# Kernel tuning notes

Measured on AMD Instinct MI355X. Metric: run time of the kernel, lower is better.

Reference implementation:

```python
import jax, jax.numpy as jnp
from jax import lax
import numpy as np

CONF_THRESH = 0.015
NMS_DIST = 4
BORDER = 4
RED = 8


def setup_inputs() -> dict:
    key = jax.random.key(0)
    k1, k2, k3, k4, k5 = jax.random.split(key, 5)
    B, C, H, W = 32, 128, 64, 64
    MID, NCLS = 256, RED * RED + 1
    return {
        "x": jax.random.normal(k1, (B, C, H, W), dtype=jnp.float32),
        "w1": jax.random.normal(k2, (MID, C, 3, 3), dtype=jnp.float32) * 0.05,
        "b1": jax.random.normal(k3, (MID,), dtype=jnp.float32) * 0.05,
        "w2": jax.random.normal(k4, (NCLS, MID, 1, 1), dtype=jnp.float32) * 0.05,
        "b2": jax.random.normal(k5, (NCLS,), dtype=jnp.float32) * 0.05,
    }


def _conv3x3(x, w, b):
    y = lax.conv_general_dilated(
        x, w, window_strides=(1, 1), padding="SAME",
        dimension_numbers=("NCHW", "OIHW", "NCHW"))
    return y + b[None, :, None, None]


def _max_pool(s, r):
    # s: [B, H, W]; infinity-norm neighborhood max, window (2r+1)x(2r+1)
    return lax.reduce_window(
        s, -jnp.inf, lax.max,
        window_dimensions=(1, 2 * r + 1, 2 * r + 1),
        window_strides=(1, 1, 1), padding="SAME")


def _grid_nms(scores, r, iters=8):
    # Iterated local-max suppression; converges to the greedy (sorted-by-score)
    # grid NMS of the original nms_fast routine for distinct scores.
    zeros = jnp.zeros_like(scores)
    max_mask = (scores == _max_pool(scores, r)) & (scores > 0)
    for _ in range(iters):
        supp = _max_pool(max_mask.astype(scores.dtype), r) > 0
        supp_scores = jnp.where(supp, zeros, scores)
        new_max = (supp_scores == _max_pool(supp_scores, r)) & (supp_scores > 0)
        max_mask = max_mask | (new_max & ~supp)
    return jnp.where(max_mask, scores, zeros)


def reference(x, w1, b1, w2, b2):
    B, _, hh, ww = x.shape
    h = jax.nn.relu(_conv3x3(x, w1, b1))                       # [B, mid, hh, ww]
    semi = jnp.einsum("bchw,oc->bohw", h, w2[:, :, 0, 0]) + b2[None, :, None, None]
    dense = jax.nn.softmax(semi, axis=1)                        # [B, 65, hh, ww]
    nodust = dense[:, :-1]                                      # drop dust bin
    # depth-to-space: [B,64,hh,ww] -> [B, hh*8, ww*8]
    heat = nodust.transpose(0, 2, 3, 1).reshape(B, hh, ww, RED, RED)
    heat = heat.transpose(0, 1, 3, 2, 4).reshape(B, hh * RED, ww * RED)
    # confidence threshold
    scores = jnp.where(heat >= CONF_THRESH, heat, 0.0)
    # grid-based NMS (dense keep-map formulation of nms_fast)
    kept = _grid_nms(scores, NMS_DIST)
    # border removal
    Hi, Wi = hh * RED, ww * RED
    yy = jnp.arange(Hi)
    xx = jnp.arange(Wi)
    border = ((yy[:, None] >= BORDER) & (yy[:, None] < Hi - BORDER) &
              (xx[None, :] >= BORDER) & (xx[None, :] < Wi - BORDER))
    return kept * border[None, :, :].astype(kept.dtype)
```

## Files before the change

### kernel.cpp

```cpp
#include <hip/hip_runtime.h>
#include <hip/hip_bf16.h>
#include <stdint.h>

#define BATCH 32
#define CIN 128
#define HH 64
#define WW 64
#define MID 256
#define NCLS 65
#define HI 512
#define NWORDS 8
#define XPS 136
#define HBS2 264
#define SEMS 68

typedef _Float16 half8 __attribute__((ext_vector_type(8)));
typedef _Float16 half4v __attribute__((ext_vector_type(4)));
typedef _Float16 half2v __attribute__((ext_vector_type(2)));
typedef float f32x4 __attribute__((ext_vector_type(4)));

__global__ __launch_bounds__(256) void prep_w1f(
    const float* __restrict__ w1, _Float16* __restrict__ w1fh,
    _Float16* __restrict__ w1fl)
{
    const int idx = blockIdx.x * 256 + threadIdx.x;
    const int j = idx & 7, lane = (idx >> 3) & 63, mt = (idx >> 9) & 15;
    const int s = (idx >> 13) & 3, kix = idx >> 15;
    const int m = mt * 16 + (lane & 15);
    const int c = s * 32 + (lane >> 4) * 8 + j;
    const int ky = kix / 3, kx = kix - ky * 3;
    const float v = w1[((m * CIN + c) * 3 + ky) * 3 + kx];
    const _Float16 hi = (_Float16)v;
    w1fh[idx] = hi;
    w1fl[idx] = (_Float16)(v - (float)hi);
}

__global__ __launch_bounds__(256) void prep_w2f(
    const float* __restrict__ w2, _Float16* __restrict__ w2fh,
    _Float16* __restrict__ w2fl)
{
    const int idx = blockIdx.x * 256 + threadIdx.x;
    const int j = idx & 7, lane = (idx >> 3) & 63;
    const int ks = (idx >> 9) & 7, mt = idx >> 12;
    const int o = mt * 16 + (lane & 15);
    const int k = ks * 32 + (lane >> 4) * 8 + j;
    const float v = (o < NCLS) ? w2[o * MID + k] : 0.f;
    const _Float16 hi = (_Float16)v;
    w2fh[idx] = hi;
    w2fl[idx] = (_Float16)(v - (float)hi);
}

__global__ __launch_bounds__(256) void head_kernel(
    const float* __restrict__ x,
    const _Float16* __restrict__ w1fh, const _Float16* __restrict__ w1fl,
    const _Float16* __restrict__ w2fh, const _Float16* __restrict__ w2fl,
    const float* __restrict__ b1, const float* __restrict__ b2,
    float* __restrict__ out)
{
    const int b  = blockIdx.z;
    const int y0 = blockIdx.y * 8, x0 = blockIdx.x * 8;
    const int tid = threadIdx.x;
    const int lane = tid & 63, w = tid >> 6;
    const int n = lane & 15, q = lane >> 4;

    __shared__ __align__(16) unsigned char SM[54400];
    _Float16* const xh = (_Float16*)SM;
    _Float16* const xl = xh + 100 * XPS;
    _Float16* const hbh = (_Float16*)SM;
    _Float16* const hbl = hbh + 32 * HBS2;
    float* const sem  = (float*)(SM + 33792);
    float* const rinv = sem + 32 * SEMS;

    const float* xb = x + (size_t)b * CIN * HH * WW;
    for (int i = tid; i < 6400; i += 256) {
        const int c2 = i / 100, pos = i - c2 * 100;
        const int r = pos / 10, cc = pos - r * 10;
        const int gy = y0 - 1 + r, gx = x0 - 1 + cc;
        const int c = c2 * 2;
        float v0 = 0.f, v1 = 0.f;
        if ((unsigned)gy < HH && (unsigned)gx < WW) {
            const float* p = xb + (c * HH + gy) * WW + gx;
            v0 = p[0]; v1 = p[HH * WW];
        }
        const _Float16 h0 = (_Float16)v0, h1 = (_Float16)v1;
        half2v hi = {h0, h1};
        half2v lo = {(_Float16)(v0 - (float)h0), (_Float16)(v1 - (float)h1)};
        *(half2v*)(xh + pos * XPS + c) = hi;
        *(half2v*)(xl + pos * XPS + c) = lo;
    }
    __syncthreads();

    f32x4 acc[4][4];
#pragma unroll
    for (int i = 0; i < 4; ++i)
#pragma unroll
        for (int t = 0; t < 4; ++t) acc[i][t] = (f32x4){0.f, 0.f, 0.f, 0.f};

    int bposT[4];
#pragma unroll
    for (int t = 0; t < 4; ++t)
        bposT[t] = (t * 2 + (n >> 3)) * 10 + (n & 7);

    for (int kix = 0; kix < 9; ++kix) {
        const int ky = kix / 3;
        const int koff = ky * 10 + (kix - ky * 3);
#pragma unroll
        for (int s = 0; s < 4; ++s) {
            half8 Ah[4], Al[4];
#pragma unroll
            for (int i = 0; i < 4; ++i) {
                const size_t o = (size_t)(kix * 4 + s) * 8192 +
                                 (w * 4 + i) * 512 + lane * 8;
                Ah[i] = *(const half8*)(w1fh + o);
                Al[i] = *(const half8*)(w1fl + o);
            }
            half8 Bh[4], Bl[4];
#pragma unroll
            for (int t = 0; t < 4; ++t) {
                const int a = (bposT[t] + koff) * XPS + s * 32 + q * 8;
                Bh[t] = *(const half8*)(xh + a);
                Bl[t] = *(const half8*)(xl + a);
            }
#pragma unroll
            for (int i = 0; i < 4; ++i)
#pragma unroll
                for (int t = 0; t < 4; ++t) {
                    acc[i][t] = __builtin_amdgcn_mfma_f32_16x16x32_f16(
                        Ah[i], Bh[t], acc[i][t], 0, 0, 0);
                    acc[i][t] = __builtin_amdgcn_mfma_f32_16x16x32_f16(
                        Ah[i], Bl[t], acc[i][t], 0, 0, 0);
                    acc[i][t] = __builtin_amdgcn_mfma_f32_16x16x32_f16(
                        Al[i], Bh[t], acc[i][t], 0, 0, 0);
                }
        }
    }
    __syncthreads();

    for (int hf = 0; hf < 2; ++hf) {
        if (hf) __syncthreads();
#pragma unroll
        for (int i = 0; i < 4; ++i)
#pragma unroll
            for (int tt = 0; tt < 2; ++tt) {
                const int t = hf * 2 + tt;
                const int p = tt * 16 + n;
                const int m0 = w * 64 + i * 16 + q * 4;
                const f32x4 a = acc[i][t];
                const float4 bv = *(const float4*)(b1 + m0);
                const float h0 = fmaxf(a[0] + bv.x, 0.f);
                const float h1 = fmaxf(a[1] + bv.y, 0.f);
                const float h2 = fmaxf(a[2] + bv.z, 0.f);
                const float h3 = fmaxf(a[3] + bv.w, 0.f);
                half4v hh = {(_Float16)h0, (_Float16)h1,
                             (_Float16)h2, (_Float16)h3};
                half4v hl = {(_Float16)(h0 - (float)hh[0]),
                             (_Float16)(h1 - (float)hh[1]),
                             (_Float16)(h2 - (float)hh[2]),
                             (_Float16)(h3 - (float)hh[3])};
                *(half4v*)(hbh + p * HBS2 + m0) = hh;
                *(half4v*)(hbl + p * HBS2 + m0) = hl;
            }
        __syncthreads();
        {
            const int nt = w & 1;
            const int mt0 = (w < 2) ? 0 : 3;
            const int nmt = (w < 2) ? 3 : 2;
            const int pb = nt * 16 + n;
            f32x4 a2[3];
#pragma unroll
            for (int j = 0; j < 3; ++j) a2[j] = (f32x4){0.f, 0.f, 0.f, 0.f};
#pragma unroll
            for (int ks = 0; ks < 8; ++ks) {
                const int ad = pb * HBS2 + ks * 32 + q * 8;
                const half8 B2h = *(const half8*)(hbh + ad);
                const half8 B2l = *(const half8*)(hbl + ad);
#pragma unroll
                for (int j = 0; j < 3; ++j)
                    if (j < nmt) {
                        const size_t o = (size_t)((mt0 + j) * 8 + ks) * 512 +
                                         lane * 8;
                        const half8 A2h = *(const half8*)(w2fh + o);
                        const half8 A2l = *(const half8*)(w2fl + o);
                        a2[j] = __builtin_amdgcn_mfma_f32_16x16x32_f16(
                            A2h, B2h, a2[j], 0, 0, 0);
                        a2[j] = __builtin_amdgcn_mfma_f32_16x16x32_f16(
                            A2h, B2l, a2[j], 0, 0, 0);
                        a2[j] = __builtin_amdgcn_mfma_f32_16x16x32_f16(
                            A2l, B2h, a2[j], 0, 0, 0);
                    }
            }
#pragma unroll
            for (int j = 0; j < 3; ++j)
                if (j < nmt) {
                    const int o0 = (mt0 + j) * 16 + q * 4;
#pragma unroll
                    for (int r2 = 0; r2 < 4; ++r2) {
                        const int o = o0 + r2;
                        if (o < NCLS)
                            sem[pb * SEMS + o] = a2[j][r2] + b2[o];
                    }
                }
        }
        __syncthreads();
        if (tid < 128) {
            const int p = tid >> 2, q4 = tid & 3;
            const int o0 = q4 * 17;
            const int o1 = (o0 + 17 < NCLS) ? o0 + 17 : NCLS;
            float mx = -1e30f;
            for (int o = o0; o < o1; ++o)
                mx = fmaxf(mx, sem[p * SEMS + o]);
            mx = fmaxf(mx, __shfl_xor(mx, 1));
            mx = fmaxf(mx, __shfl_xor(mx, 2));
            float ssum = 0.f;
            for (int o = o0; o < o1; ++o) {
                float e = __expf(sem[p * SEMS + o] - mx);
                sem[p * SEMS + o] = e;
                ssum += e;
            }
            ssum += __shfl_xor(ssum, 1);
            ssum += __shfl_xor(ssum, 2);
            if (q4 == 0) rinv[p] = 1.f / ssum;
        }
        __syncthreads();
        for (int t2 = tid; t2 < 2048; t2 += 256) {
            const int p = t2 >> 6, o = t2 & 63;
            float v = sem[p * SEMS + o] * rinv[p];
            if (!(v >= 0.015f)) v = 0.f;
            const int P = hf * 32 + p;
            const int py = P >> 3, px = P & 7;
            const int row = (y0 + py) * 8 + (o >> 3);
            const int col = (x0 + px) * 8 + (o & 7);
            out[((size_t)b * HI + row) * HI + col] = v;
        }
    }
}

__global__ __launch_bounds__(256) void nms_iter(
    const float* __restrict__ S, const uint64_t* __restrict__ Min,
    uint64_t* __restrict__ Mout)
{
    const int b = blockIdx.z;
    const int bx = blockIdx.x;
    const int ty = blockIdx.y * 64, tx = bx * 64;
    const int tid = threadIdx.x;

    __shared__ uint64_t smw[80 * 3];
    __shared__ uint64_t hd[80 * 3];
    __shared__ uint64_t sup[72 * 3];
    __shared__ __align__(16) float sfl[72 * 76];
    __shared__ __align__(16) float rm[72 * 64];

    if (tid < 240) {
        const int i = tid / 3, j = tid % 3;
        const int yy = ty - 8 + i;
        const int wj = bx - 1 + j;
        uint64_t v = 0;
        if (Min && (unsigned)yy < HI && (unsigned)wj < NWORDS)
            v = Min[((size_t)b * HI + yy) * NWORDS + wj];
        smw[tid] = v;
    }
    __syncthreads();
    if (tid < 240) {
        const int i = tid / 3, j = tid % 3;
        const uint64_t c = smw[i * 3 + j];
        const uint64_t l = j > 0 ? smw[i * 3 + j - 1] : 0ull;
        const uint64_t r = j < 2 ? smw[i * 3 + j + 1] : 0ull;
        uint64_t d = c;
#pragma unroll
        for (int s = 1; s <= 4; ++s)
            d |= (c >> s) | (r << (64 - s)) | (c << s) | (l >> (64 - s));
        hd[tid] = d;
    }
    __syncthreads();
    if (tid < 216) {
        const int r = tid / 3, j = tid % 3;
        uint64_t v = 0;
#pragma unroll
        for (int k = 0; k < 9; ++k) v |= hd[(r + k) * 3 + j];
        sup[tid] = v;
    }
    __syncthreads();
    const float* Sb = S + (size_t)b * HI * HI;
    for (int k = tid; k < 72 * 18; k += 256) {
        const int r = k / 18, f4 = k % 18;
        const int gy = ty - 4 + r;
        const int gx0 = tx - 4 + f4 * 4;
        float4 v = make_float4(0.f, 0.f, 0.f, 0.f);
        float* pv = (float*)&v;
        if ((unsigned)gy < HI) {
            if (gx0 >= 0 && gx0 + 3 < HI)
                v = *(const float4*)(Sb + (size_t)gy * HI + gx0);
            else {
#pragma unroll
                for (int cc = 0; cc < 4; ++cc)
                    if ((unsigned)(gx0 + cc) < HI)
                        pv[cc] = Sb[(size_t)gy * HI + gx0 + cc];
            }
        }
        const int rel64 = 60 + 4 * f4;
        const uint64_t w = sup[r * 3 + (rel64 >> 6)];
        const int b0 = rel64 & 63;
#pragma unroll
        for (int cc = 0; cc < 4; ++cc)
            if ((w >> (b0 + cc)) & 1ull) pv[cc] = 0.f;
        *(float4*)(sfl + r * 76 + f4 * 4) = v;
    }
    __syncthreads();
    for (int k = tid; k < 72 * 16; k += 256) {
        const int r = k / 16, x4 = (k % 16) * 4;
        const float4 a  = *(const float4*)(sfl + r * 76 + x4);
        const float4 bq = *(const float4*)(sfl + r * 76 + x4 + 4);
        const float4 cq = *(const float4*)(sfl + r * 76 + x4 + 8);
        const float v0=a.x,v1=a.y,v2=a.z,v3=a.w;
        const float v4=bq.x,v5=bq.y,v6=bq.z,v7=bq.w;
        const float v8=cq.x,v9=cq.y,v10=cq.z,v11=cq.w;
        const float m4567 = fmaxf(fmaxf(v4,v5), fmaxf(v6,v7));
        const float m23 = fmaxf(v2,v3), m89 = fmaxf(v8,v9);
        const float o0 = fmaxf(fmaxf(fmaxf(v0,v1), m23), fmaxf(m4567, v8));
        const float o1 = fmaxf(fmaxf(v1, m23), fmaxf(m4567, m89));
        const float o2 = fmaxf(fmaxf(m23, m4567), fmaxf(m89, v10));
        const float o3 = fmaxf(fmaxf(v3, m4567), fmaxf(fmaxf(m89, v10), v11));
        *(float4*)(rm + r * 64 + x4) = make_float4(o0,o1,o2,o3);
    }
    __syncthreads();
    {
        const int wv = tid >> 6, lane = tid & 63;
        const int ybase = wv * 16;
        float ring[9];
#pragma unroll
        for (int k = 0; k < 8; ++k) ring[k] = rm[(ybase + k) * 64 + lane];
#pragma unroll
        for (int qq = 0; qq < 16; ++qq) {
            const int y = ybase + qq;
            ring[(qq + 8) % 9] = rm[(y + 8) * 64 + lane];
            float mv = ring[0];
#pragma unroll
            for (int k = 1; k < 9; ++k) mv = fmaxf(mv, ring[k]);
            const float c = sfl[(y + 4) * 76 + lane + 4];
            const uint64_t oldw = smw[(y + 8) * 3 + 1];
            const bool keep = ((oldw >> lane) & 1ull) || (c == mv && c > 0.f);
            const uint64_t word = __ballot(keep);
            if (lane == 0)
                Mout[((size_t)b * HI + ty + y) * NWORDS + bx] = word;
        }
    }
}

__global__ __launch_bounds__(256) void finalize_bits(
    float* __restrict__ S, const uint64_t* __restrict__ Mw)
{
    const int i4 = blockIdx.x * 256 + threadIdx.x;
    const size_t base = (size_t)i4 * 4;
    const int x = (int)(base & 511);
    const int y = (int)((base >> 9) & 511);
    const int bb = (int)(base >> 18);
    const uint64_t w = Mw[((size_t)bb * HI + y) * NWORDS + (x >> 6)];
    float4 v = ((const float4*)S)[i4];
    float* pv = (float*)&v;
    const bool rowok = (y >= 4) && (y < HI - 4);
#pragma unroll
    for (int cc = 0; cc < 4; ++cc) {
        const int xx = x + cc;
        const bool keep = rowok && (xx >= 4) && (xx < HI - 4) &&
                          ((w >> (xx & 63)) & 1ull);
        if (!keep) pv[cc] = 0.f;
    }
    ((float4*)S)[i4] = v;
}

extern "C" void kernel_launch(void* const* d_in, const int* in_sizes, int n_in,
                              void* d_out, int out_size, void* d_ws, size_t ws_size,
                              hipStream_t stream) {
    const float* x  = (const float*)d_in[0];
    const float* w1 = (const float*)d_in[1];
    const float* b1 = (const float*)d_in[2];
    const float* w2 = (const float*)d_in[3];
    const float* b2 = (const float*)d_in[4];
    float* out = (float*)d_out;

    char* wsb = (char*)d_ws;
    _Float16* w1fh = (_Float16*)(wsb);
    _Float16* w1fl = (_Float16*)(wsb + 0x90000);
    _Float16* w2fh = (_Float16*)(wsb + 0x120000);
    _Float16* w2fl = (_Float16*)(wsb + 0x130000);
    uint64_t* MA   = (uint64_t*)(wsb + 0x140000);
    uint64_t* MB   = (uint64_t*)(wsb + 0x240000);

    prep_w1f<<<294912 / 256, 256, 0, stream>>>(w1, w1fh, w1fl);
    prep_w2f<<<20480 / 256, 256, 0, stream>>>(w2, w2fh, w2fl);
    head_kernel<<<dim3(8, 8, BATCH), 256, 0, stream>>>(
        x, w1fh, w1fl, w2fh, w2fl, b1, b2, out);

    dim3 g(NWORDS, 8, BATCH);
    nms_iter<<<g, 256, 0, stream>>>(out, nullptr, MA);
    for (int it = 0; it < 4; ++it) {
        nms_iter<<<g, 256, 0, stream>>>(out, MA, MB);
        nms_iter<<<g, 256, 0, stream>>>(out, MB, MA);
    }
    const int nf4 = BATCH * HI * HI / 4;
    finalize_bits<<<nf4 / 256, 256, 0, stream>>>(out, MA);
}
```

Baseline: 597.3 us.

## Shrink head LDS footprint via channel chunking and skip converged NMS iterations

The head kernel now stages the input tile in two 64-channel chunks and runs the second 1x1 conv and softmax in four 16-position slices. This cuts shared memory use from about 54KB to about 29KB so more blocks can be resident per CU, at the cost of extra barriers and fewer waves taking part in the second conv. The NMS iterations now set a global change flag, and once a pass produces no change, later launches only copy the mask words and return early. The early exit keeps the result identical to the fixed iteration count, but every launch still runs and has to read the flag.

```diff
diff --git a/kernel.cpp b/kernel.cpp
--- a/kernel.cpp
+++ b/kernel.cpp
@@ -10,7 +10,7 @@
 #define NCLS 65
 #define HI 512
 #define NWORDS 8
-#define XPS 136
+#define XP2 72
 #define HBS2 264
 #define SEMS 68
 
@@ -21,9 +21,10 @@
 
 __global__ __launch_bounds__(256) void prep_w1f(
     const float* __restrict__ w1, _Float16* __restrict__ w1fh,
-    _Float16* __restrict__ w1fl)
+    _Float16* __restrict__ w1fl, int* __restrict__ flags)
 {
     const int idx = blockIdx.x * 256 + threadIdx.x;
+    if (blockIdx.x == 0 && threadIdx.x < 16) flags[threadIdx.x] = 0;
     const int j = idx & 7, lane = (idx >> 3) & 63, mt = (idx >> 9) & 15;
     const int s = (idx >> 13) & 3, kix = idx >> 15;
     const int m = mt * 16 + (lane & 15);
@@ -63,32 +64,15 @@
     const int lane = tid & 63, w = tid >> 6;
     const int n = lane & 15, q = lane >> 4;
 
-    __shared__ __align__(16) unsigned char SM[54400];
+    __shared__ __align__(16) unsigned char SM[28800];
     _Float16* const xh = (_Float16*)SM;
-    _Float16* const xl = xh + 100 * XPS;
+    _Float16* const xl = xh + 100 * XP2;
     _Float16* const hbh = (_Float16*)SM;
-    _Float16* const hbl = hbh + 32 * HBS2;
-    float* const sem  = (float*)(SM + 33792);
-    float* const rinv = sem + 32 * SEMS;
+    _Float16* const hbl = hbh + 16 * HBS2;
+    float* const sem  = (float*)(SM + 16896);
+    float* const rinv = sem + 16 * SEMS;
 
     const float* xb = x + (size_t)b * CIN * HH * WW;
-    for (int i = tid; i < 6400; i += 256) {
-        const int c2 = i / 100, pos = i - c2 * 100;
-        const int r = pos / 10, cc = pos - r * 10;
-        const int gy = y0 - 1 + r, gx = x0 - 1 + cc;
-        const int c = c2 * 2;
-        float v0 = 0.f, v1 = 0.f;
-        if ((unsigned)gy < HH && (unsigned)gx < WW) {
-            const float* p = xb + (c * HH + gy) * WW + gx;
-            v0 = p[0]; v1 = p[HH * WW];
-        }
-        const _Float16 h0 = (_Float16)v0, h1 = (_Float16)v1;
-        half2v hi = {h0, h1};
-        half2v lo = {(_Float16)(v0 - (float)h0), (_Float16)(v1 - (float)h1)};
-        *(half2v*)(xh + pos * XPS + c) = hi;
-        *(half2v*)(xl + pos * XPS + c) = lo;
-    }
-    __syncthreads();
 
     f32x4 acc[4][4];
 #pragma unroll
@@ -101,108 +85,126 @@
     for (int t = 0; t < 4; ++t)
         bposT[t] = (t * 2 + (n >> 3)) * 10 + (n & 7);
 
-    for (int kix = 0; kix < 9; ++kix) {
-        const int ky = kix / 3;
-        const int koff = ky * 10 + (kix - ky * 3);
-#pragma unroll
-        for (int s = 0; s < 4; ++s) {
-            half8 Ah[4], Al[4];
-#pragma unroll
-            for (int i = 0; i < 4; ++i) {
-                const size_t o = (size_t)(kix * 4 + s) * 8192 +
-                                 (w * 4 + i) * 512 + lane * 8;
-                Ah[i] = *(const half8*)(w1fh + o);
-                Al[i] = *(const half8*)(w1fl + o);
-            }
-            half8 Bh[4], Bl[4];
-#pragma unroll
-            for (int t = 0; t < 4; ++t) {
-                const int a = (bposT[t] + koff) * XPS + s * 32 + q * 8;
-                Bh[t] = *(const half8*)(xh + a);
-                Bl[t] = *(const half8*)(xl + a);
-            }
-#pragma unroll
-            for (int i = 0; i < 4; ++i)
+    for (int ch = 0; ch < 2; ++ch) {
+        __syncthreads();
+        for (int i = tid; i < 3200; i += 256) {
+            const int c2 = i / 100, pos = i - c2 * 100;
+            const int r = pos / 10, cc = pos - r * 10;
+            const int gy = y0 - 1 + r, gx = x0 - 1 + cc;
+            const int cg = ch * 64 + c2 * 2;
+            float v0 = 0.f, v1 = 0.f;
+            if ((unsigned)gy < HH && (unsigned)gx < WW) {
+                const float* p = xb + (cg * HH + gy) * WW + gx;
+                v0 = p[0]; v1 = p[HH * WW];
+            }
+            const _Float16 h0 = (_Float16)v0, h1 = (_Float16)v1;
+            half2v hi = {h0, h1};
+            half2v lo = {(_Float16)(v0 - (float)h0),
+                         (_Float16)(v1 - (float)h1)};
+            *(half2v*)(xh + pos * XP2 + c2 * 2) = hi;
+            *(half2v*)(xl + pos * XP2 + c2 * 2) = lo;
+        }
+        __syncthreads();
+        for (int kix = 0; kix < 9; ++kix) {
+            const int ky = kix / 3;
+            const int koff = ky * 10 + (kix - ky * 3);
+#pragma unroll
+            for (int s2 = 0; s2 < 2; ++s2) {
+                const int s = ch * 2 + s2;
+                half8 Ah[4], Al[4];
+#pragma unroll
+                for (int i = 0; i < 4; ++i) {
+                    const size_t o = (size_t)(kix * 4 + s) * 8192 +
+                                     (w * 4 + i) * 512 + lane * 8;
+                    Ah[i] = *(const half8*)(w1fh + o);
+                    Al[i] = *(const half8*)(w1fl + o);
+                }
+                half8 Bh[4], Bl[4];
 #pragma unroll
                 for (int t = 0; t < 4; ++t) {
-                    acc[i][t] = __builtin_amdgcn_mfma_f32_16x16x32_f16(
-                        Ah[i], Bh[t], acc[i][t], 0, 0, 0);
-                    acc[i][t] = __builtin_amdgcn_mfma_f32_16x16x32_f16(
-                        Ah[i], Bl[t], acc[i][t], 0, 0, 0);
-                    acc[i][t] = __builtin_amdgcn_mfma_f32_16x16x32_f16(
-                        Al[i], Bh[t], acc[i][t], 0, 0, 0);
+                    const int a = (bposT[t] + koff) * XP2 + s2 * 32 + q * 8;
+                    Bh[t] = *(const half8*)(xh + a);
+                    Bl[t] = *(const half8*)(xl + a);
                 }
-        }
-    }
-    __syncthreads();
-
-    for (int hf = 0; hf < 2; ++hf) {
-        if (hf) __syncthreads();
-#pragma unroll
-        for (int i = 0; i < 4; ++i)
-#pragma unroll
-            for (int tt = 0; tt < 2; ++tt) {
-                const int t = hf * 2 + tt;
-                const int p = tt * 16 + n;
-                const int m0 = w * 64 + i * 16 + q * 4;
-                const f32x4 a = acc[i][t];
-                const float4 bv = *(const float4*)(b1 + m0);
-                const float h0 = fmaxf(a[0] + bv.x, 0.f);
-                const float h1 = fmaxf(a[1] + bv.y, 0.f);
-                const float h2 = fmaxf(a[2] + bv.z, 0.f);
-                const float h3 = fmaxf(a[3] + bv.w, 0.f);
-                half4v hh = {(_Float16)h0, (_Float16)h1,
-                             (_Float16)h2, (_Float16)h3};
-                half4v hl = {(_Float16)(h0 - (float)hh[0]),
-                             (_Float16)(h1 - (float)hh[1]),
-                             (_Float16)(h2 - (float)hh[2]),
-                             (_Float16)(h3 - (float)hh[3])};
-                *(half4v*)(hbh + p * HBS2 + m0) = hh;
-                *(half4v*)(hbl + p * HBS2 + m0) = hl;
-            }
+#pragma unroll
+                for (int i = 0; i < 4; ++i)
+#pragma unroll
+                    for (int t = 0; t < 4; ++t) {
+                        acc[i][t] = __builtin_amdgcn_mfma_f32_16x16x32_f16(
+                            Ah[i], Bh[t], acc[i][t], 0, 0, 0);
+                        acc[i][t] = __builtin_amdgcn_mfma_f32_16x16x32_f16(
+                            Ah[i], Bl[t], acc[i][t], 0, 0, 0);
+                        acc[i][t] = __builtin_amdgcn_mfma_f32_16x16x32_f16(
+                            Al[i], Bh[t], acc[i][t], 0, 0, 0);
+                    }
+            }
+        }
+    }
+
+    for (int t = 0; t < 4; ++t) {
+        __syncthreads();
+#pragma unroll
+        for (int i = 0; i < 4; ++i) {
+            const int m0 = w * 64 + i * 16 + q * 4;
+            const f32x4 a = acc[i][t];
+            const float4 bv = *(const float4*)(b1 + m0);
+            const float h0 = fmaxf(a[0] + bv.x, 0.f);
+            const float h1 = fmaxf(a[1] + bv.y, 0.f);
+            const float h2 = fmaxf(a[2] + bv.z, 0.f);
+            const float h3 = fmaxf(a[3] + bv.w, 0.f);
+            half4v hh = {(_Float16)h0, (_Float16)h1,
+                         (_Float16)h2, (_Float16)h3};
+            half4v hl = {(_Float16)(h0 - (float)hh[0]),
+                         (_Float16)(h1 - (float)hh[1]),
+                         (_Float16)(h2 - (float)hh[2]),
+                         (_Float16)(h3 - (float)hh[3])};
+            *(half4v*)(hbh + n * HBS2 + m0) = hh;
+            *(half4v*)(hbl + n * HBS2 + m0) = hl;
+        }
         __syncthreads();
         {
-            const int nt = w & 1;
-            const int mt0 = (w < 2) ? 0 : 3;
-            const int nmt = (w < 2) ? 3 : 2;
-            const int pb = nt * 16 + n;
-            f32x4 a2[3];
-#pragma unroll
-            for (int j = 0; j < 3; ++j) a2[j] = (f32x4){0.f, 0.f, 0.f, 0.f};
-#pragma unroll
-            for (int ks = 0; ks < 8; ++ks) {
-                const int ad = pb * HBS2 + ks * 32 + q * 8;
-                const half8 B2h = *(const half8*)(hbh + ad);
-                const half8 B2l = *(const half8*)(hbl + ad);
-#pragma unroll
-                for (int j = 0; j < 3; ++j)
-                    if (j < nmt) {
-                        const size_t o = (size_t)((mt0 + j) * 8 + ks) * 512 +
-                                         lane * 8;
-                        const half8 A2h = *(const half8*)(w2fh + o);
-                        const half8 A2l = *(const half8*)(w2fl + o);
-                        a2[j] = __builtin_amdgcn_mfma_f32_16x16x32_f16(
-                            A2h, B2h, a2[j], 0, 0, 0);
-                        a2[j] = __builtin_amdgcn_mfma_f32_16x16x32_f16(
-                            A2h, B2l, a2[j], 0, 0, 0);
-                        a2[j] = __builtin_amdgcn_mfma_f32_16x16x32_f16(
-                            A2l, B2h, a2[j], 0, 0, 0);
+            const int mtbase = (w == 0) ? 0 : (w == 1) ? 2 : (w == 2) ? 4 : 5;
+            const int mtcnt  = (w < 2) ? 2 : (w == 2) ? 1 : 0;
+            f32x4 a2[2];
+            a2[0] = (f32x4){0.f, 0.f, 0.f, 0.f};
+            a2[1] = (f32x4){0.f, 0.f, 0.f, 0.f};
+            if (mtcnt) {
+#pragma unroll
+                for (int ks = 0; ks < 8; ++ks) {
+                    const int ad = n * HBS2 + ks * 32 + q * 8;
+                    const half8 B2h = *(const half8*)(hbh + ad);
+                    const half8 B2l = *(const half8*)(hbl + ad);
+#pragma unroll
+                    for (int j = 0; j < 2; ++j)
+                        if (j < mtcnt) {
+                            const size_t o =
+                                (size_t)((mtbase + j) * 8 + ks) * 512 +
+                                lane * 8;
+                            const half8 A2h = *(const half8*)(w2fh + o);
+                            const half8 A2l = *(const half8*)(w2fl + o);
+                            a2[j] = __builtin_amdgcn_mfma_f32_16x16x32_f16(
+                                A2h, B2h, a2[j], 0, 0, 0);
+                            a2[j] = __builtin_amdgcn_mfma_f32_16x16x32_f16(
+                                A2h, B2l, a2[j], 0, 0, 0);
+                            a2[j] = __builtin_amdgcn_mfma_f32_16x16x32_f16(
+                                A2l, B2h, a2[j], 0, 0, 0);
+                        }
+                }
+#pragma unroll
+                for (int j = 0; j < 2; ++j)
+                    if (j < mtcnt) {
+                        const int o0 = (mtbase + j) * 16 + q * 4;
+#pragma unroll
+                        for (int r2 = 0; r2 < 4; ++r2) {
+                            const int o = o0 + r2;
+                            if (o < NCLS)
+                                sem[n * SEMS + o] = a2[j][r2] + b2[o];
+                        }
                     }
             }
-#pragma unroll
-            for (int j = 0; j < 3; ++j)
-                if (j < nmt) {
-                    const int o0 = (mt0 + j) * 16 + q * 4;
-#pragma unroll
-                    for (int r2 = 0; r2 < 4; ++r2) {
-                        const int o = o0 + r2;
-                        if (o < NCLS)
-                            sem[pb * SEMS + o] = a2[j][r2] + b2[o];
-                    }
-                }
-        }
-        __syncthreads();
-        if (tid < 128) {
+        }
+        __syncthreads();
+        if (tid < 64) {
             const int p = tid >> 2, q4 = tid & 3;
             const int o0 = q4 * 17;
             const int o1 = (o0 + 17 < NCLS) ? o0 + 17 : NCLS;
@@ -222,11 +224,11 @@
             if (q4 == 0) rinv[p] = 1.f / ssum;
         }
         __syncthreads();
-        for (int t2 = tid; t2 < 2048; t2 += 256) {
+        for (int t2 = tid; t2 < 1024; t2 += 256) {
             const int p = t2 >> 6, o = t2 & 63;
             float v = sem[p * SEMS + o] * rinv[p];
             if (!(v >= 0.015f)) v = 0.f;
-            const int P = hf * 32 + p;
+            const int P = t * 16 + p;
             const int py = P >> 3, px = P & 7;
             const int row = (y0 + py) * 8 + (o >> 3);
             const int col = (x0 + px) * 8 + (o & 7);
@@ -237,19 +239,30 @@
 
 __global__ __launch_bounds__(256) void nms_iter(
     const float* __restrict__ S, const uint64_t* __restrict__ Min,
-    uint64_t* __restrict__ Mout)
+    uint64_t* __restrict__ Mout, const int* __restrict__ flagIn,
+    int* __restrict__ flagOut)
 {
     const int b = blockIdx.z;
     const int bx = blockIdx.x;
     const int ty = blockIdx.y * 64, tx = bx * 64;
     const int tid = threadIdx.x;
 
+    if (flagIn && flagIn[0] == 0) {
+        if (tid < 64) {
+            const size_t idx = ((size_t)b * HI + ty + tid) * NWORDS + bx;
+            Mout[idx] = Min[idx];
+        }
+        return;
+    }
+
     __shared__ uint64_t smw[80 * 3];
     __shared__ uint64_t hd[80 * 3];
     __shared__ uint64_t sup[72 * 3];
     __shared__ __align__(16) float sfl[72 * 76];
     __shared__ __align__(16) float rm[72 * 64];
-
+    __shared__ int schg;
+
+    if (tid == 0) schg = 0;
     if (tid < 240) {
         const int i = tid / 3, j = tid % 3;
         const int yy = ty - 8 + i;
@@ -326,6 +339,7 @@
     {
         const int wv = tid >> 6, lane = tid & 63;
         const int ybase = wv * 16;
+        bool chg = false;
         float ring[9];
 #pragma unroll
         for (int k = 0; k < 8; ++k) ring[k] = rm[(ybase + k) * 64 + lane];
@@ -340,10 +354,15 @@
             const uint64_t oldw = smw[(y + 8) * 3 + 1];
             const bool keep = ((oldw >> lane) & 1ull) || (c == mv && c > 0.f);
             const uint64_t word = __ballot(keep);
-            if (lane == 0)
+            if (lane == 0) {
                 Mout[((size_t)b * HI + ty + y) * NWORDS + bx] = word;
-        }
-    }
+                chg |= (word != oldw);
+            }
+        }
+        if (lane == 0 && chg) schg = 1;
+    }
+    __syncthreads();
+    if (tid == 0 && schg) atomicOr(flagOut, 1);
 }
 
 __global__ __launch_bounds__(256) void finalize_bits(
@@ -385,18 +404,19 @@
     _Float16* w2fl = (_Float16*)(wsb + 0x130000);
     uint64_t* MA   = (uint64_t*)(wsb + 0x140000);
     uint64_t* MB   = (uint64_t*)(wsb + 0x240000);
-
-    prep_w1f<<<294912 / 256, 256, 0, stream>>>(w1, w1fh, w1fl);
+    int* flags     = (int*)(wsb + 0x340000);
+
+    prep_w1f<<<294912 / 256, 256, 0, stream>>>(w1, w1fh, w1fl, flags);
     prep_w2f<<<20480 / 256, 256, 0, stream>>>(w2, w2fh, w2fl);
     head_kernel<<<dim3(8, 8, BATCH), 256, 0, stream>>>(
         x, w1fh, w1fl, w2fh, w2fl, b1, b2, out);
 
     dim3 g(NWORDS, 8, BATCH);
-    nms_iter<<<g, 256, 0, stream>>>(out, nullptr, MA);
-    for (int it = 0; it < 4; ++it) {
-        nms_iter<<<g, 256, 0, stream>>>(out, MA, MB);
-        nms_iter<<<g, 256, 0, stream>>>(out, MB, MA);
-    }
+    uint64_t* bufs[2] = {MA, MB};
+    nms_iter<<<g, 256, 0, stream>>>(out, nullptr, MA, nullptr, flags + 0);
+    for (int it = 1; it <= 8; ++it)
+        nms_iter<<<g, 256, 0, stream>>>(out, bufs[(it + 1) & 1], bufs[it & 1],
+                                        flags + it - 1, flags + it);
     const int nf4 = BATCH * HI * HI / 4;
     finalize_bits<<<nf4 / 256, 256, 0, stream>>>(out, MA);
 }
```

Result: slower. 680.1 us (+13.9%).
